# Kernel tuning notes

Hardware: AMD Instinct MI355X
Metric: run time of the kernel (lower is better)

## Reference

```python
import jax, jax.numpy as jnp
import numpy as np

NEG_SLOPE = 0.01  # torch LeakyReLU default
EPS = 1e-5        # torch BatchNorm2d default
N_BINS = 17       # quantization indices 0..16 for uniform [0,1) input


def _bn(x, g, b):
    # training-mode BatchNorm2d: biased batch stats over (B, H, W) per channel
    m = jnp.mean(x, axis=(0, 2, 3), keepdims=True)
    v = jnp.var(x, axis=(0, 2, 3), keepdims=True)
    return (x - m) * jax.lax.rsqrt(v + EPS) * g[None, :, None, None] + b[None, :, None, None]


def _lrelu(x):
    return jnp.where(x >= 0, x, NEG_SLOPE * x)


def _mode_pool_11(idx):
    # idx: int32 (B,C,H,W) quantization bin indices; 11x11 reflect-padded sliding-window mode.
    # Histogram formulation: one-hot over N_BINS, box-sum via 2D integral image, argmax.
    # argmax takes the FIRST max -> smallest modal value, matching torch.mode tie-breaking.
    k = jnp.pad(idx, ((0, 0), (0, 0), (5, 5), (5, 5)), mode='reflect')
    oh = (k[..., None] == jnp.arange(N_BINS, dtype=jnp.int32)).astype(jnp.float32)  # (B,C,Hp,Wp,17)
    I = jnp.cumsum(jnp.cumsum(oh, axis=2), axis=3)
    I = jnp.pad(I, ((0, 0), (0, 0), (1, 0), (1, 0), (0, 0)))
    cnt = I[:, :, 11:, 11:] - I[:, :, :-11, 11:] - I[:, :, 11:, :-11] + I[:, :, :-11, :-11]
    return jnp.argmax(cnt, axis=-1)  # (B,C,H,W) int


def _nearest(x, H, W):
    # torch F.interpolate mode='nearest': src = floor(dst * in / out)
    h, w = x.shape[2], x.shape[3]
    ri = (jnp.arange(H) * h) // H
    ci = (jnp.arange(W) * w) // W
    return x[:, :, ri][:, :, :, ci]


def _conv1x1(x, w, b):
    return jnp.einsum('bchw,oc->bohw', x, w) + b[None, :, None, None]


def reference(x, pw1, pb1, g1, be1, pw2, pb2, g2, be2, dw, sw, gs, bs):
    B, C, H, W = x.shape
    half = pw1.shape[0]
    # quantize: (x*255/16).round() * 16/256 -> index path (round has zero grad anyway)
    idx = jnp.round(x * 255.0 / 16.0).astype(jnp.int32)
    xq = _mode_pool_11(idx).astype(x.dtype) * (16.0 / 256.0)
    # prepare: conv1x1 -> BN -> LeakyReLU, twice
    h1 = _lrelu(_bn(_conv1x1(xq, pw1, pb1), g1, be1))
    prep = _lrelu(_bn(_conv1x1(h1, pw2, pb2), g2, be2))
    score = jnp.zeros((B, 2 * half, H, W), dtype=x.dtype)
    dn = ('NCHW', 'OIHW', 'NCHW')
    previous = prep
    d = prep
    # static pyramid: 512 -> 171 -> 57 -> 19 -> 7 -> 3 -> 1 (shapes known at trace time)
    while min(d.shape[2], d.shape[3]) >= 3:
        d = jax.lax.conv_general_dilated(d, dw, (3, 3), ((1, 1), (1, 1)), dimension_numbers=dn)
        z = _nearest(d, H, W)
        # interleave previous/zoomout per channel: ch 2c=prev[c], 2c+1=zoom[c]
        mix = jnp.stack([previous, z], axis=2).reshape(B, 2 * half, H, W)
        previous = z
        # grouped 1x1 conv: groups=half, 2 in / 2 out channels per group, no bias
        sc = jnp.einsum('bgihw,goi->bgohw', mix.reshape(B, half, 2, H, W), sw).reshape(B, 2 * half, H, W)
        score = score + _lrelu(_bn(sc, gs, bs))
    return score


def setup_inputs() -> dict:
    key = jax.random.key(0)
    ks = jax.random.split(key, 6)
    B, C, H, W = 8, 3, 512, 512
    half = 16
    x = jax.random.uniform(ks[0], (B, C, H, W), dtype=jnp.float32)
    pw1 = 0.1 * jax.random.normal(ks[1], (half, C), dtype=jnp.float32)
    pb1 = jnp.zeros((half,), jnp.float32)
    g1 = jnp.ones((half,), jnp.float32)
    be1 = jnp.zeros((half,), jnp.float32)
    pw2 = 0.1 * jax.random.normal(ks[2], (half, half), dtype=jnp.float32)
    pb2 = jnp.zeros((half,), jnp.float32)
    g2 = jnp.ones((half,), jnp.float32)
    be2 = jnp.zeros((half,), jnp.float32)
    dw = 0.1 * jax.random.normal(ks[3], (half, half, 3, 3), dtype=jnp.float32)
    sw = 0.1 * jax.random.normal(ks[4], (half, 2, 2), dtype=jnp.float32)
    gs = jnp.ones((2 * half,), jnp.float32)
    bs = jnp.zeros((2 * half,), jnp.float32)
    return {'x': x, 'pw1': pw1, 'pb1': pb1, 'g1': g1, 'be1': be1,
            'pw2': pw2, 'pb2': pb2, 'g2': g2, 'be2': be2,
            'dw': dw, 'sw': sw, 'gs': gs, 'bs': bs}
```

## Files before the change

### kernel.cpp

```cpp
#include <hip/hip_runtime.h>
#include <stdint.h>


#define NPX   2097152
#define NINV  (1.0f/2097152.0f)

#define OFF_STATS 0
#define OFF_HIST  16384
#define OFF_LUT   36864
#define OFF_MODE  194560
#define OFF_D1    73594880
#define OFF_D2    88566272
#define OFF_D3    90229760
#define OFF_D4    90414592
#define OFF_D5    90439680
#define OFF_D6    90444288

#define S_PRE1    0
#define S2_PRE1   16
#define S_H1      32
#define S_H1H1    48
#define S_PREP    184
#define S2_PREP   200
#define S_Z1      216
#define S2_Z1     232
#define S_PZ1     248
#define S_LVLBASE 264
#define P_A1      512
#define P_B1      560
#define P_A2      576
#define P_B2      832
#define P_AFF     848

__device__ __forceinline__ uint32_t f2bf(float f) {
  uint32_t u = __float_as_uint(f);
  u += 0x7FFFu + ((u >> 16) & 1u);
  return u >> 16;
}
__device__ __forceinline__ float bf2f(uint32_t u) {
  return __uint_as_float(u << 16);
}

__device__ __forceinline__ float wave_red(float v) {
  v += __shfl_down(v, 32); v += __shfl_down(v, 16); v += __shfl_down(v, 8);
  v += __shfl_down(v, 4);  v += __shfl_down(v, 2);  v += __shfl_down(v, 1);
  return v;
}

template<int K, bool ATOMIC>
__device__ __forceinline__ void block_red(float* acc, float* dst, float* lds) {
  int lane = threadIdx.x & 63, wid = threadIdx.x >> 6;
#pragma unroll
  for (int k = 0; k < K; ++k) {
    float v = wave_red(acc[k]);
    if (lane == 0) lds[wid * K + k] = v;
  }
  __syncthreads();
  if ((int)threadIdx.x < K) {
    float s = lds[threadIdx.x] + lds[K + threadIdx.x] + lds[2 * K + threadIdx.x] + lds[3 * K + threadIdx.x];
    if (ATOMIC) atomicAdd(&dst[threadIdx.x], s);
    else        dst[threadIdx.x] = s;
  }
}

__global__ __launch_bounds__(256) void k_mode(const float* __restrict__ x,
                                              uint8_t* __restrict__ mode) {
  int bx = blockIdx.x;
  int rb = bx & 15, cb = (bx >> 4) & 1, pl = bx >> 5;
  __shared__ uint8_t tile[42][272];
  const float* xp = x + (size_t)pl * 262144;
  int tid = threadIdx.x;
  for (int e = tid; e < 42 * 266; e += 256) {
    int lr = e / 266, lc = e - lr * 266;
    int gr = rb * 32 - 5 + lr; if (gr < 0) gr = -gr; else if (gr > 511) gr = 1022 - gr;
    int gc = cb * 256 - 5 + lc; if (gc < 0) gc = -gc; else if (gc > 511) gc = 1022 - gc;
    float v = xp[gr * 512 + gc];
    tile[lr][lc] = (uint8_t)(int)rintf((v * 255.0f) * 0.0625f);
  }
  __syncthreads();
  int t = tid;
  uint32_t h0 = 0, h1 = 0, h2 = 0, h3 = 0, h4 = 0;
#define ADDV(vv) { int v_ = (vv); uint32_t inc_ = 1u << ((v_ & 3) << 3); int w_ = v_ >> 2; \
    h0 += (w_ == 0) ? inc_ : 0u; h1 += (w_ == 1) ? inc_ : 0u; h2 += (w_ == 2) ? inc_ : 0u; \
    h3 += (w_ == 3) ? inc_ : 0u; h4 += (w_ == 4) ? inc_ : 0u; }
#define SUBV(vv) { int v_ = (vv); uint32_t inc_ = 1u << ((v_ & 3) << 3); int w_ = v_ >> 2; \
    h0 -= (w_ == 0) ? inc_ : 0u; h1 -= (w_ == 1) ? inc_ : 0u; h2 -= (w_ == 2) ? inc_ : 0u; \
    h3 -= (w_ == 3) ? inc_ : 0u; h4 -= (w_ == 4) ? inc_ : 0u; }
#define SCAN_STORE(OI) { uint32_t best_ = h0 & 255u; int bi_ = 0; uint32_t c_; \
    c_ = (h0 >> 8)  & 255u; if (c_ > best_) { best_ = c_; bi_ = 1; } \
    c_ = (h0 >> 16) & 255u; if (c_ > best_) { best_ = c_; bi_ = 2; } \
    c_ = (h0 >> 24);        if (c_ > best_) { best_ = c_; bi_ = 3; } \
    c_ = h1 & 255u;         if (c_ > best_) { best_ = c_; bi_ = 4; } \
    c_ = (h1 >> 8)  & 255u; if (c_ > best_) { best_ = c_; bi_ = 5; } \
    c_ = (h1 >> 16) & 255u; if (c_ > best_) { best_ = c_; bi_ = 6; } \
    c_ = (h1 >> 24);        if (c_ > best_) { best_ = c_; bi_ = 7; } \
    c_ = h2 & 255u;         if (c_ > best_) { best_ = c_; bi_ = 8; } \
    c_ = (h2 >> 8)  & 255u; if (c_ > best_) { best_ = c_; bi_ = 9; } \
    c_ = (h2 >> 16) & 255u; if (c_ > best_) { best_ = c_; bi_ = 10; } \
    c_ = (h2 >> 24);        if (c_ > best_) { best_ = c_; bi_ = 11; } \
    c_ = h3 & 255u;         if (c_ > best_) { best_ = c_; bi_ = 12; } \
    c_ = (h3 >> 8)  & 255u; if (c_ > best_) { best_ = c_; bi_ = 13; } \
    c_ = (h3 >> 16) & 255u; if (c_ > best_) { best_ = c_; bi_ = 14; } \
    c_ = (h3 >> 24);        if (c_ > best_) { best_ = c_; bi_ = 15; } \
    c_ = h4 & 255u;         if (c_ > best_) { best_ = c_; bi_ = 16; } \
    mode[OI] = (uint8_t)bi_; }
#pragma unroll
  for (int dy = 0; dy < 11; ++dy) {
#pragma unroll
    for (int dx = 0; dx < 11; ++dx) ADDV(tile[dy][t + dx]);
  }
  size_t ob = (size_t)pl * 262144 + (size_t)(rb * 32) * 512 + cb * 256 + t;
  SCAN_STORE(ob);
  for (int s = 1; s < 32; ++s) {
#pragma unroll
    for (int dx = 0; dx < 11; ++dx) { SUBV(tile[s - 1][t + dx]); ADDV(tile[s + 10][t + dx]); }
    SCAN_STORE(ob + (size_t)s * 512);
  }
#undef ADDV
#undef SUBV
#undef SCAN_STORE
}

__global__ __launch_bounds__(256) void k_hist(const uint8_t* __restrict__ mode,
                                              uint32_t* __restrict__ hist) {
  __shared__ uint32_t h[4913];
  int tid = threadIdx.x;
  for (int e = tid; e < 4913; e += 256) h[e] = 0;
  __syncthreads();
  int base = blockIdx.x * 8192;
  for (int it = 0; it < 16; ++it) {
    int px = base + it * 512 + tid * 2;
    int b = px >> 18, rem = px & 262143;
    const uint8_t* mp = mode + (size_t)b * 786432 + rem;
    uint32_t m0 = *(const uint16_t*)(mp);
    uint32_t m1 = *(const uint16_t*)(mp + 262144);
    uint32_t m2 = *(const uint16_t*)(mp + 524288);
    int c0 = (int)(m0 & 255u) + 17 * (int)(m1 & 255u) + 289 * (int)(m2 & 255u);
    int c1 = (int)(m0 >> 8)   + 17 * (int)(m1 >> 8)   + 289 * (int)(m2 >> 8);
    atomicAdd(&h[c0], 1u);
    atomicAdd(&h[c1], 1u);
  }
  __syncthreads();
  for (int e = tid; e < 4913; e += 256)
    if (h[e]) atomicAdd(&hist[e], h[e]);
}

__global__ __launch_bounds__(256) void k_build(const uint32_t* __restrict__ hist,
    const float* __restrict__ pw1, const float* __restrict__ pb1,
    const float* __restrict__ g1,  const float* __restrict__ be1,
    const float* __restrict__ pw2, const float* __restrict__ pb2,
    const float* __restrict__ g2,  const float* __restrict__ be2,
    float* __restrict__ stats, uint32_t* __restrict__ lut) {
  __shared__ float red[4 * 152];
  int tid = threadIdx.x;
  {
    float acc[32];
#pragma unroll
    for (int k = 0; k < 32; ++k) acc[k] = 0.f;
    for (int bin = tid; bin < 4913; bin += 256) {
      float w = (float)hist[bin];
      if (w == 0.f) continue;
      int m0 = bin % 17, r = bin / 17;
      int m1 = r % 17, m2 = r / 17;
      float x0 = m0 * 0.0625f, x1 = m1 * 0.0625f, x2 = m2 * 0.0625f;
#pragma unroll
      for (int o = 0; o < 16; ++o) {
        float p = fmaf(pw1[o * 3], x0, fmaf(pw1[o * 3 + 1], x1, fmaf(pw1[o * 3 + 2], x2, pb1[o])));
        acc[o] = fmaf(w, p, acc[o]);
        acc[16 + o] = fmaf(w * p, p, acc[16 + o]);
      }
    }
    block_red<32, false>(acc, stats + S_PRE1, red);
  }
  __syncthreads();
  if (tid < 16) {
    int o = tid;
    float m = stats[S_PRE1 + o] * NINV;
    float var = stats[S2_PRE1 + o] * NINV - m * m;
    float s = g1[o] * rsqrtf(var + 1e-5f);
    stats[P_A1 + o * 3 + 0] = pw1[o * 3 + 0] * s;
    stats[P_A1 + o * 3 + 1] = pw1[o * 3 + 1] * s;
    stats[P_A1 + o * 3 + 2] = pw1[o * 3 + 2] * s;
    stats[P_B1 + o] = (pb1[o] - m) * s + be1[o];
  }
  __syncthreads();
  {
    float acc[152];
#pragma unroll
    for (int k = 0; k < 152; ++k) acc[k] = 0.f;
    for (int bin = tid; bin < 4913; bin += 256) {
      float w = (float)hist[bin];
      if (w == 0.f) continue;
      int m0 = bin % 17, r = bin / 17;
      int m1 = r % 17, m2 = r / 17;
      float x0 = m0 * 0.0625f, x1 = m1 * 0.0625f, x2 = m2 * 0.0625f;
      float h[16];
#pragma unroll
      for (int c = 0; c < 16; ++c) {
        float y = fmaf(stats[P_A1 + c * 3], x0, fmaf(stats[P_A1 + c * 3 + 1], x1,
                  fmaf(stats[P_A1 + c * 3 + 2], x2, stats[P_B1 + c])));
        h[c] = fmaxf(y, 0.01f * y);
        acc[c] = fmaf(w, h[c], acc[c]);
      }
#pragma unroll
      for (int c = 0; c < 16; ++c) {
#pragma unroll
        for (int c2 = c; c2 < 16; ++c2) {
          int idx = 16 * c - (c * (c - 1)) / 2 + (c2 - c);
          acc[16 + idx] = fmaf(w * h[c], h[c2], acc[16 + idx]);
        }
      }
    }
    block_red<152, false>(acc, stats + S_H1, red);
  }
  __syncthreads();
  if (tid < 16) {
    int o = tid;
    float s1 = 0.f;
#pragma unroll
    for (int c = 0; c < 16; ++c) s1 = fmaf(pw2[o * 16 + c], stats[S_H1 + c] * NINV, s1);
    float e2 = 0.f;
#pragma unroll
    for (int c = 0; c < 16; ++c) {
#pragma unroll
      for (int c2 = 0; c2 < 16; ++c2) {
        int lo = c < c2 ? c : c2, hi = c < c2 ? c2 : c;
        int idx = 16 * lo - (lo * (lo - 1)) / 2 + (hi - lo);
        e2 = fmaf(pw2[o * 16 + c] * pw2[o * 16 + c2], stats[S_H1H1 + idx] * NINV, e2);
      }
    }
    float var = e2 - s1 * s1;
    float mean = s1 + pb2[o];
    float s = g2[o] * rsqrtf(var + 1e-5f);
#pragma unroll
    for (int c = 0; c < 16; ++c) stats[P_A2 + o * 16 + c] = pw2[o * 16 + c] * s;
    stats[P_B2 + o] = (pb2[o] - mean) * s + be2[o];
  }
  __syncthreads();
  {
    float acc[32];
#pragma unroll
    for (int k = 0; k < 32; ++k) acc[k] = 0.f;
    for (int bin = tid; bin < 4913; bin += 256) {
      float w = (float)hist[bin];
      int m0 = bin % 17, r = bin / 17;
      int m1 = r % 17, m2 = r / 17;
      float x0 = m0 * 0.0625f, x1 = m1 * 0.0625f, x2 = m2 * 0.0625f;
      float h[16];
#pragma unroll
      for (int c = 0; c < 16; ++c) {
        float y = fmaf(stats[P_A1 + c * 3], x0, fmaf(stats[P_A1 + c * 3 + 1], x1,
                  fmaf(stats[P_A1 + c * 3 + 2], x2, stats[P_B1 + c])));
        h[c] = fmaxf(y, 0.01f * y);
      }
      float p[16];
#pragma unroll
      for (int o = 0; o < 16; ++o) {
        float y = stats[P_B2 + o];
#pragma unroll
        for (int c = 0; c < 16; ++c) y = fmaf(stats[P_A2 + o * 16 + c], h[c], y);
        p[o] = fmaxf(y, 0.01f * y);
        acc[o] = fmaf(w, p[o], acc[o]);
        acc[16 + o] = fmaf(w * p[o], p[o], acc[16 + o]);
      }
#pragma unroll
      for (int d = 0; d < 8; ++d)
        lut[bin * 8 + d] = f2bf(p[2 * d]) | (f2bf(p[2 * d + 1]) << 16);
    }
    block_red<32, false>(acc, stats + S_PREP, red);
  }
}

template<int HIN, int WIN, int HOUT, int WOUT>
__device__ __forceinline__ void conv_body(const float* __restrict__ in,
                                          float* __restrict__ out,
                                          const float* __restrict__ dw, int bx) {
  __shared__ float tile[3][16][WIN + 2];
  int r = bx % HOUT, b = bx / HOUT;
  int tid = threadIdx.x;
  for (int e = tid; e < 48; e += 256) { tile[e / 16][e & 15][0] = 0.f; tile[e / 16][e & 15][WIN + 1] = 0.f; }
  for (int e = tid; e < 3 * 16 * WIN; e += 256) {
    int ky = e / (16 * WIN); int rem = e - ky * (16 * WIN); int ic = rem / WIN; int col = rem - ic * WIN;
    int gr = 3 * r - 1 + ky;
    float v = 0.f;
    if (gr >= 0 && gr < HIN) v = in[((size_t)(b * 16 + ic) * HIN + gr) * WIN + col];
    tile[ky][ic][col + 1] = v;
  }
  __syncthreads();
  int c = tid;
  if (c < WOUT) {
    float acc[16];
#pragma unroll
    for (int o = 0; o < 16; ++o) acc[o] = 0.f;
#pragma unroll
    for (int ic = 0; ic < 16; ++ic) {
      float v[9];
#pragma unroll
      for (int ky = 0; ky < 3; ++ky) {
#pragma unroll
        for (int kx = 0; kx < 3; ++kx) v[ky * 3 + kx] = tile[ky][ic][3 * c + kx];
      }
#pragma unroll
      for (int o = 0; o < 16; ++o) {
        const float* w = dw + (o * 16 + ic) * 9;
#pragma unroll
        for (int tp = 0; tp < 9; ++tp) acc[o] = fmaf(v[tp], w[tp], acc[o]);
      }
    }
#pragma unroll
    for (int o = 0; o < 16; ++o)
      out[((size_t)(b * 16 + o) * HOUT + r) * WOUT + c] = acc[o];
  }
}

template<int HP, int HZ>
__device__ __forceinline__ void pair_body(const float* __restrict__ dp,
                                          const float* __restrict__ dz,
                                          float* __restrict__ dst, int bx) {
  int g = bx & 15, b = (bx >> 4) & 7, jq = bx >> 7;
  const float* dpp = dp + (size_t)(b * 16 + g) * HP * HP;
  const float* dzp = dz + (size_t)(b * 16 + g) * HZ * HZ;
  float a1 = 0.f, a2 = 0.f, a3 = 0.f;
  for (int j = jq * 128; j < jq * 128 + 128; ++j) {
    int r1 = (j * HP) >> 9, r2 = (j * HZ) >> 9;
    const float* rp = dpp + r1 * HP;
    const float* rz = dzp + r2 * HZ;
    for (int i = threadIdx.x; i < 512; i += 256) {
      int c1 = (i * HP) >> 9, c2 = (i * HZ) >> 9;
      float zp = rp[c1], zz = rz[c2];
      a1 += zz; a2 = fmaf(zz, zz, a2); a3 = fmaf(zp, zz, a3);
    }
  }
  a1 = wave_red(a1); a2 = wave_red(a2); a3 = wave_red(a3);
  __shared__ float red[12];
  int lane = threadIdx.x & 63, wid = threadIdx.x >> 6;
  if (!lane) { red[wid * 3] = a1; red[wid * 3 + 1] = a2; red[wid * 3 + 2] = a3; }
  __syncthreads();
  if (threadIdx.x < 3) {
    float s = red[threadIdx.x] + red[3 + threadIdx.x] + red[6 + threadIdx.x] + red[9 + threadIdx.x];
    atomicAdd(&dst[threadIdx.x * 16 + g], s);
  }
}

__device__ __forceinline__ void corr1_body(const uint8_t* __restrict__ mode,
                                           const uint32_t* __restrict__ lut,
                                           const float* __restrict__ d1,
                                           float* __restrict__ stats, int bx) {
  int b = bx >> 6, band = bx & 63;
  float acc[48];
#pragma unroll
  for (int k = 0; k < 48; ++k) acc[k] = 0.f;
  for (int jj = 0; jj < 8; ++jj) {
    int j = band * 8 + jj;
    int r1 = (j * 171) >> 9;
#pragma unroll
    for (int ii = 0; ii < 2; ++ii) {
      int i = (int)threadIdx.x + ii * 256;
      int c1 = (i * 171) >> 9;
      const uint8_t* mp = mode + (size_t)b * 786432 + j * 512 + i;
      int combo = (int)mp[0] + 17 * (int)mp[262144] + 289 * (int)mp[524288];
      const uint4* L = (const uint4*)(lut + combo * 8);
      uint4 q0 = L[0], q1 = L[1];
      uint32_t q[8] = {q0.x, q0.y, q0.z, q0.w, q1.x, q1.y, q1.z, q1.w};
#pragma unroll
      for (int g = 0; g < 16; ++g) {
        float p = bf2f((g & 1) ? (q[g >> 1] >> 16) : (q[g >> 1] & 0xFFFFu));
        float z = d1[((size_t)(b * 16 + g) * 171 + r1) * 171 + c1];
        acc[g] += z; acc[16 + g] = fmaf(z, z, acc[16 + g]); acc[32 + g] = fmaf(p, z, acc[32 + g]);
      }
    }
  }
  __shared__ float red[4 * 48];
  block_red<48, true>(acc, stats + S_Z1, red);
}

__global__ __launch_bounds__(256) void k_conv1g(const uint8_t* __restrict__ mode,
                                                const uint32_t* __restrict__ lut,
                                                float* __restrict__ out,
                                                const float* __restrict__ dw) {
  __shared__ uint16_t tile[3][16][514];
  int bx = blockIdx.x; int r = bx % 171, b = bx / 171;
  int tid = threadIdx.x;
  for (int e = tid; e < 48; e += 256) { tile[e / 16][e & 15][0] = 0; tile[e / 16][e & 15][513] = 0; }
  for (int e = tid; e < 3 * 512; e += 256) {
    int ky = e >> 9, col = e & 511;
    int gr = 3 * r - 1 + ky;
    if (gr < 0 || gr > 511) {
#pragma unroll
      for (int c = 0; c < 16; ++c) tile[ky][c][col + 1] = 0;
    } else {
      const uint8_t* mp = mode + (size_t)b * 786432 + gr * 512 + col;
      int combo = (int)mp[0] + 17 * (int)mp[262144] + 289 * (int)mp[524288];
      const uint4* L = (const uint4*)(lut + combo * 8);
      uint4 q0 = L[0], q1 = L[1];
      uint32_t q[8] = {q0.x, q0.y, q0.z, q0.w, q1.x, q1.y, q1.z, q1.w};
#pragma unroll
      for (int d = 0; d < 8; ++d) {
        tile[ky][2 * d][col + 1]     = (uint16_t)(q[d] & 0xFFFFu);
        tile[ky][2 * d + 1][col + 1] = (uint16_t)(q[d] >> 16);
      }
    }
  }
  __syncthreads();
  int c = tid;
  if (c < 171) {
    float acc[16];
#pragma unroll
    for (int o = 0; o < 16; ++o) acc[o] = 0.f;
#pragma unroll
    for (int ic = 0; ic < 16; ++ic) {
      float v[9];
#pragma unroll
      for (int ky = 0; ky < 3; ++ky) {
#pragma unroll
        for (int kx = 0; kx < 3; ++kx)
          v[ky * 3 + kx] = __uint_as_float(((uint32_t)tile[ky][ic][3 * c + kx]) << 16);
      }
#pragma unroll
      for (int o = 0; o < 16; ++o) {
        const float* w = dw + (o * 16 + ic) * 9;
#pragma unroll
        for (int tp = 0; tp < 9; ++tp) acc[o] = fmaf(v[tp], w[tp], acc[o]);
      }
    }
#pragma unroll
    for (int o = 0; o < 16; ++o)
      out[((size_t)(b * 16 + o) * 171 + r) * 171 + c] = acc[o];
  }
}

__global__ __launch_bounds__(256) void k_conv2_corr1(const float* __restrict__ d1,
    float* __restrict__ d2, const float* __restrict__ dw,
    const uint8_t* __restrict__ mode, const uint32_t* __restrict__ lut,
    float* __restrict__ stats) {
  if ((int)blockIdx.x < 456) conv_body<171, 171, 57, 57>(d1, d2, dw, (int)blockIdx.x);
  else                       corr1_body(mode, lut, d1, stats, (int)blockIdx.x - 456);
}

template<int HIN, int WIN, int HOUT, int WOUT, int NCONV, int HP, int HZ>
__global__ __launch_bounds__(256) void k_conv_pair(const float* __restrict__ cin,
    float* __restrict__ cout, const float* __restrict__ dw,
    const float* __restrict__ dp, const float* __restrict__ dz,
    float* __restrict__ dst) {
  if ((int)blockIdx.x < NCONV) conv_body<HIN, WIN, HOUT, WOUT>(cin, cout, dw, (int)blockIdx.x);
  else                         pair_body<HP, HZ>(dp, dz, dst, (int)blockIdx.x - NCONV);
}

__global__ __launch_bounds__(256) void k_bnL2(float* stats, const float* __restrict__ sw,
    const float* __restrict__ gs, const float* __restrict__ bs,
    const float* __restrict__ d5, const float* __restrict__ d6) {
  __shared__ float l6[3][16][8];
  int t = threadIdx.x;
  if (t < 128) {
    int b = t >> 4, g = t & 15;
    float z6 = d6[b * 16 + g];
    const float* z5 = d5 + (size_t)(b * 16 + g) * 9;
    const float wr[3] = {171.f, 171.f, 170.f};
    float s5 = 0.f;
#pragma unroll
    for (int r = 0; r < 3; ++r)
#pragma unroll
      for (int c = 0; c < 3; ++c) s5 = fmaf(wr[r] * wr[c], z5[r * 3 + c], s5);
    l6[0][g][b] = z6; l6[1][g][b] = z6 * z6; l6[2][g][b] = z6 * s5;
  }
  __syncthreads();
  if (t < 48) {
    int w = t >> 4, g = t & 15;
    float s = 0.f;
#pragma unroll
    for (int b = 0; b < 8; ++b) s += l6[w][g][b];
    stats[S_LVLBASE + 4 * 48 + w * 16 + g] = (w == 2) ? s : s * 262144.f;
  }
  __syncthreads();
  if (t < 192) {
    int lvl = t >> 5, ch = t & 31, g = ch >> 1, o = ch & 1;
    float Sp, Sp2, Sz, Sz2, Spz;
    if (lvl == 0) {
      Sp = stats[S_PREP + g]; Sp2 = stats[S2_PREP + g];
      Sz = stats[S_Z1 + g];   Sz2 = stats[S2_Z1 + g]; Spz = stats[S_PZ1 + g];
    } else {
      int base = S_LVLBASE + (lvl - 1) * 48;
      Sz = stats[base + g]; Sz2 = stats[base + 16 + g]; Spz = stats[base + 32 + g];
      if (lvl == 1) { Sp = stats[S_Z1 + g]; Sp2 = stats[S2_Z1 + g]; }
      else { int pb = S_LVLBASE + (lvl - 2) * 48; Sp = stats[pb + g]; Sp2 = stats[pb + 16 + g]; }
    }
    float mp = Sp * NINV, mz = Sz * NINV;
    float ep2 = Sp2 * NINV, ez2 = Sz2 * NINV, epz = Spz * NINV;
    float w0 = sw[g * 4 + o * 2], w1 = sw[g * 4 + o * 2 + 1];
    float mean = w0 * mp + w1 * mz;
    float e2 = w0 * w0 * ep2 + 2.f * w0 * w1 * epz + w1 * w1 * ez2;
    float var = e2 - mean * mean;
    float s = gs[ch] * rsqrtf(var + 1e-5f);
    float* a = stats + P_AFF + (lvl * 32 + ch) * 3;
    a[0] = s * w0; a[1] = s * w1; a[2] = bs[ch] - mean * s;
  }
}

__global__ __launch_bounds__(256) void k_score(const uint8_t* __restrict__ mode,
    const uint32_t* __restrict__ lut,
    const float* __restrict__ d1, const float* __restrict__ d2, const float* __restrict__ d3,
    const float* __restrict__ d4, const float* __restrict__ d5, const float* __restrict__ d6,
    const float* __restrict__ stats, float* __restrict__ out) {
  __shared__ float zrow[4128];
  __shared__ float aff[576];
  __shared__ uint16_t prow[16][512];
  int bx = blockIdx.x; int b = bx >> 9, j = bx & 511;
  int tid = threadIdx.x;
  {
    const uint8_t* mp = mode + (size_t)b * 786432 + j * 512 + tid * 2;
    uint32_t m0 = *(const uint16_t*)(mp);
    uint32_t m1 = *(const uint16_t*)(mp + 262144);
    uint32_t m2 = *(const uint16_t*)(mp + 524288);
    int ca = (int)(m0 & 255u) + 17 * (int)(m1 & 255u) + 289 * (int)(m2 & 255u);
    int cb = (int)(m0 >> 8)   + 17 * (int)(m1 >> 8)   + 289 * (int)(m2 >> 8);
    const uint4* La = (const uint4*)(lut + ca * 8);
    const uint4* Lb = (const uint4*)(lut + cb * 8);
    uint4 a0 = La[0], a1 = La[1], b0 = Lb[0], b1 = Lb[1];
    uint32_t pa[8] = {a0.x, a0.y, a0.z, a0.w, a1.x, a1.y, a1.z, a1.w};
    uint32_t pb[8] = {b0.x, b0.y, b0.z, b0.w, b1.x, b1.y, b1.z, b1.w};
    uint32_t* pr32 = (uint32_t*)prow;
#pragma unroll
    for (int c = 0; c < 16; ++c) {
      uint32_t lo = (c & 1) ? (pa[c >> 1] >> 16)         : (pa[c >> 1] & 0xFFFFu);
      uint32_t hi = (c & 1) ? (pb[c >> 1] & 0xFFFF0000u) : (pb[c >> 1] << 16);
      pr32[c * 256 + tid] = lo | hi;
    }
  }
  for (int e = tid; e < 576; e += 256) aff[e] = stats[P_AFF + e];
  { int r = (j * 171) >> 9; for (int e = tid; e < 16 * 171; e += 256) { int g = e / 171, c = e - g * 171; zrow[e]        = d1[((size_t)(b * 16 + g) * 171 + r) * 171 + c]; } }
  { int r = (j * 57)  >> 9; for (int e = tid; e < 16 * 57;  e += 256) { int g = e / 57,  c = e - g * 57;  zrow[2736 + e] = d2[((size_t)(b * 16 + g) * 57  + r) * 57  + c]; } }
  { int r = (j * 19)  >> 9; for (int e = tid; e < 16 * 19;  e += 256) { int g = e / 19,  c = e - g * 19;  zrow[3648 + e] = d3[((size_t)(b * 16 + g) * 19  + r) * 19  + c]; } }
  { int r = (j * 7)   >> 9; for (int e = tid; e < 16 * 7;   e += 256) { int g = e / 7,   c = e - g * 7;   zrow[3952 + e] = d4[((size_t)(b * 16 + g) * 7   + r) * 7   + c]; } }
  { int r = (j * 3)   >> 9; for (int e = tid; e < 16 * 3;   e += 256) { int g = e / 3,   c = e - g * 3;   zrow[4064 + e] = d5[((size_t)(b * 16 + g) * 3   + r) * 3   + c]; } }
  { for (int e = tid; e < 16; e += 256) zrow[4112 + e] = d6[b * 16 + e]; }
  __syncthreads();
  int wave = tid >> 6, lane = tid & 63;
#pragma unroll
  for (int gi = 0; gi < 4; ++gi) {
    int g = wave * 4 + gi;
    float A[36];
#pragma unroll
    for (int l = 0; l < 6; ++l) {
#pragma unroll
      for (int q = 0; q < 6; ++q) A[l * 6 + q] = aff[(l * 32 + 2 * g) * 3 + q];
    }
    float z6 = zrow[4112 + g];
    const uint16_t* prow_g = &prow[g][0];
    float* orow = out + ((size_t)(b * 32 + 2 * g) * 512 + j) * 512;
    const float* z1p = zrow + g * 171;
    const float* z2p = zrow + 2736 + g * 57;
    const float* z3p = zrow + 3648 + g * 19;
    const float* z4p = zrow + 3952 + g * 7;
    const float* z5p = zrow + 4064 + g * 3;
#pragma unroll
    for (int k = 0; k < 4; ++k) {
      int i = (lane << 1) + (k << 7);
      uint32_t pv = *(const uint32_t*)(prow_g + i);
      float pA = bf2f(pv & 0xFFFFu), pB = bf2f(pv >> 16);
      int ib = i + 1;
      float za1 = z1p[(i * 171) >> 9], zb1 = z1p[(ib * 171) >> 9];
      float za2 = z2p[(i * 57) >> 9],  zb2 = z2p[(ib * 57) >> 9];
      float za3 = z3p[(i * 19) >> 9],  zb3 = z3p[(ib * 19) >> 9];
      float za4 = z4p[(i * 7) >> 9],   zb4 = z4p[(ib * 7) >> 9];
      float za5 = z5p[(i * 3) >> 9],   zb5 = z5p[(ib * 3) >> 9];
      float o0a = 0.f, o1a = 0.f, prevA = pA;
      float o0b = 0.f, o1b = 0.f, prevB = pB;
#define ST(L, ZA, ZB) { float y_; \
      y_ = fmaf(A[L*6+0], prevA, fmaf(A[L*6+1], (ZA), A[L*6+2])); o0a += fmaxf(y_, 0.01f * y_); \
      y_ = fmaf(A[L*6+3], prevA, fmaf(A[L*6+4], (ZA), A[L*6+5])); o1a += fmaxf(y_, 0.01f * y_); \
      y_ = fmaf(A[L*6+0], prevB, fmaf(A[L*6+1], (ZB), A[L*6+2])); o0b += fmaxf(y_, 0.01f * y_); \
      y_ = fmaf(A[L*6+3], prevB, fmaf(A[L*6+4], (ZB), A[L*6+5])); o1b += fmaxf(y_, 0.01f * y_); \
      prevA = (ZA); prevB = (ZB); }
      ST(0, za1, zb1) ST(1, za2, zb2) ST(2, za3, zb3) ST(3, za4, zb4) ST(4, za5, zb5) ST(5, z6, z6)
#undef ST
      float2 s0 = make_float2(o0a, o0b);
      float2 s1 = make_float2(o1a, o1b);
      *(float2*)(orow + i) = s0;
      *(float2*)(orow + 262144 + i) = s1;
    }
  }
}

extern "C" void kernel_launch(void* const* d_in, const int* in_sizes, int n_in,
                              void* d_out, int out_size, void* d_ws, size_t ws_size,
                              hipStream_t stream) {
  const float* x   = (const float*)d_in[0];
  const float* pw1 = (const float*)d_in[1];
  const float* pb1 = (const float*)d_in[2];
  const float* g1  = (const float*)d_in[3];
  const float* be1 = (const float*)d_in[4];
  const float* pw2 = (const float*)d_in[5];
  const float* pb2 = (const float*)d_in[6];
  const float* g2  = (const float*)d_in[7];
  const float* be2 = (const float*)d_in[8];
  const float* dw  = (const float*)d_in[9];
  const float* sw  = (const float*)d_in[10];
  const float* gs  = (const float*)d_in[11];
  const float* bs  = (const float*)d_in[12];
  char* ws = (char*)d_ws;
  float*    stats = (float*)(ws + OFF_STATS);
  uint32_t* hist  = (uint32_t*)(ws + OFF_HIST);
  uint32_t* lut   = (uint32_t*)(ws + OFF_LUT);
  uint8_t*  mode  = (uint8_t*)(ws + OFF_MODE);
  float* d1 = (float*)(ws + OFF_D1);
  float* d2 = (float*)(ws + OFF_D2);
  float* d3 = (float*)(ws + OFF_D3);
  float* d4 = (float*)(ws + OFF_D4);
  float* d5 = (float*)(ws + OFF_D5);
  float* d6 = (float*)(ws + OFF_D6);
  float* out = (float*)d_out;

  hipMemsetAsync(ws, 0, 36864, stream);
  k_mode<<<768, 256, 0, stream>>>(x, mode);
  k_hist<<<256, 256, 0, stream>>>(mode, hist);
  k_build<<<1, 256, 0, stream>>>(hist, pw1, pb1, g1, be1, pw2, pb2, g2, be2, stats, lut);
  k_conv1g<<<8 * 171, 256, 0, stream>>>(mode, lut, d1, dw);
  k_conv2_corr1<<<456 + 512, 256, 0, stream>>>(d1, d2, dw, mode, lut, stats);
  k_conv_pair<57, 57, 19, 19, 152, 171, 57><<<152 + 512, 256, 0, stream>>>(d2, d3, dw, d1, d2, stats + S_LVLBASE + 0 * 48);
  k_conv_pair<19, 19, 7, 7, 56, 57, 19><<<56 + 512, 256, 0, stream>>>(d3, d4, dw, d2, d3, stats + S_LVLBASE + 1 * 48);
  k_conv_pair<7, 7, 3, 3, 24, 19, 7><<<24 + 512, 256, 0, stream>>>(d4, d5, dw, d3, d4, stats + S_LVLBASE + 2 * 48);
  k_conv_pair<3, 3, 1, 1, 8, 7, 3><<<8 + 512, 256, 0, stream>>>(d5, d6, dw, d4, d5, stats + S_LVLBASE + 3 * 48);
  k_bnL2<<<1, 256, 0, stream>>>(stats, sw, gs, bs, d5, d6);
  k_score<<<4096, 256, 0, stream>>>(mode, lut, d1, d2, d3, d4, d5, d6, stats, out);
}
```

Baseline: 802.8 us.

## Fuse tail pyramid levels into one kernel and fold BN affine into score

Replaces the last three conv_pair launches and the single-block k_bnL2 launch with one k_tail8 kernel. In it, one block per batch runs the small 19->7->3->1 convolutions in shared memory and accumulates the level statistics with shared atomics. The final BN affine computation moves into the prologue of every k_score block, so the separate stats->affine kernel goes away. This cuts the launch count and serial dependencies at the small pyramid levels. In exchange, each of the 4096 score blocks recomputes the affine terms redundantly, and the tail convolutions run on only 8 blocks.

```diff
diff --git a/kernel.cpp b/kernel.cpp
--- a/kernel.cpp
+++ b/kernel.cpp
@@ -30,7 +30,6 @@
 #define P_B1      560
 #define P_A2      576
 #define P_B2      832
-#define P_AFF     848
 
 __device__ __forceinline__ uint32_t f2bf(float f) {
   uint32_t u = __float_as_uint(f);
@@ -437,43 +436,160 @@
   else                       corr1_body(mode, lut, d1, stats, (int)blockIdx.x - 456);
 }
 
-template<int HIN, int WIN, int HOUT, int WOUT, int NCONV, int HP, int HZ>
-__global__ __launch_bounds__(256) void k_conv_pair(const float* __restrict__ cin,
-    float* __restrict__ cout, const float* __restrict__ dw,
-    const float* __restrict__ dp, const float* __restrict__ dz,
-    float* __restrict__ dst) {
-  if ((int)blockIdx.x < NCONV) conv_body<HIN, WIN, HOUT, WOUT>(cin, cout, dw, (int)blockIdx.x);
-  else                         pair_body<HP, HZ>(dp, dz, dst, (int)blockIdx.x - NCONV);
-}
-
-__global__ __launch_bounds__(256) void k_bnL2(float* stats, const float* __restrict__ sw,
+__global__ __launch_bounds__(256) void k_conv3_pair(const float* __restrict__ d2,
+    float* __restrict__ d3, const float* __restrict__ dw,
+    const float* __restrict__ d1, float* __restrict__ stats) {
+  if ((int)blockIdx.x < 152) conv_body<57, 57, 19, 19>(d2, d3, dw, (int)blockIdx.x);
+  else                       pair_body<171, 57>(d1, d2, stats + S_LVLBASE, (int)blockIdx.x - 152);
+}
+
+__global__ __launch_bounds__(256) void k_tail8(const float* __restrict__ d2,
+    const float* __restrict__ d3, float* __restrict__ d4, float* __restrict__ d5,
+    float* __restrict__ d6, const float* __restrict__ dw, float* __restrict__ stats) {
+  int bx = blockIdx.x;
+  if (bx >= 8) { pair_body<57, 19>(d2, d3, stats + S_LVLBASE + 48, bx - 8); return; }
+  __shared__ float s3[16][19][19];
+  __shared__ float s4[16][7][7];
+  __shared__ float s5[16][3][3];
+  __shared__ float s6[16];
+  __shared__ float dwS[2304];
+  __shared__ float acc[144];
+  int tid = threadIdx.x, b = bx;
+  for (int e = tid; e < 2304; e += 256) dwS[e] = dw[e];
+  for (int e = tid; e < 144; e += 256) acc[e] = 0.f;
+  for (int e = tid; e < 16 * 361; e += 256) ((float*)s3)[e] = d3[(size_t)b * 5776 + e];
+  __syncthreads();
+  for (int e = tid; e < 784; e += 256) {
+    int o = e / 49, rc = e - o * 49; int r = rc / 7, c = rc % 7;
+    float a = 0.f;
+#pragma unroll
+    for (int ic = 0; ic < 16; ++ic) {
+      const float* w = dwS + (o * 16 + ic) * 9;
+#pragma unroll
+      for (int ky = 0; ky < 3; ++ky) {
+        int gr = 3 * r - 1 + ky; if (gr < 0 || gr > 18) continue;
+#pragma unroll
+        for (int kx = 0; kx < 3; ++kx) {
+          int gc = 3 * c - 1 + kx; if (gc < 0 || gc > 18) continue;
+          a = fmaf(s3[ic][gr][gc], w[ky * 3 + kx], a);
+        }
+      }
+    }
+    s4[o][r][c] = a; d4[((size_t)(b * 16 + o) * 7 + r) * 7 + c] = a;
+  }
+  __syncthreads();
+  for (int e = tid; e < 784; e += 256) {
+    int g = e & 15, rc = e >> 4; int r2 = rc / 7, c2 = rc % 7;
+    int loZ = (512 * r2 + 6) / 7, hiZ = (512 * (r2 + 1) + 6) / 7;
+    int loC = (512 * c2 + 6) / 7, hiC = (512 * (c2 + 1) + 6) / 7;
+    int rrmin = (loZ * 19) >> 9, rrmax = ((hiZ - 1) * 19) >> 9;
+    int ccmin = (loC * 19) >> 9, ccmax = ((hiC - 1) * 19) >> 9;
+    float z = s4[g][r2][c2];
+    float B = 0.f;
+    for (int rr = rrmin; rr <= rrmax; ++rr) {
+      int loP = (512 * rr + 18) / 19, hiP = (512 * (rr + 1) + 18) / 19;
+      int cntR = min(hiP, hiZ) - max(loP, loZ); if (cntR <= 0) continue;
+      float rowS = 0.f;
+      for (int cc = ccmin; cc <= ccmax; ++cc) {
+        int loQ = (512 * cc + 18) / 19, hiQ = (512 * (cc + 1) + 18) / 19;
+        int cntC = min(hiQ, hiC) - max(loQ, loC); if (cntC <= 0) continue;
+        rowS = fmaf((float)cntC, s3[g][rr][cc], rowS);
+      }
+      B = fmaf((float)cntR, rowS, B);
+    }
+    float wgt = (float)((hiZ - loZ) * (hiC - loC));
+    atomicAdd(&acc[g], wgt * z);
+    atomicAdd(&acc[16 + g], wgt * z * z);
+    atomicAdd(&acc[32 + g], B * z);
+  }
+  for (int e = tid; e < 144; e += 256) {
+    int o = e / 9, rc = e - o * 9; int r = rc / 3, c = rc % 3;
+    float a = 0.f;
+#pragma unroll
+    for (int ic = 0; ic < 16; ++ic) {
+      const float* w = dwS + (o * 16 + ic) * 9;
+#pragma unroll
+      for (int ky = 0; ky < 3; ++ky) {
+        int gr = 3 * r - 1 + ky; if (gr < 0 || gr > 6) continue;
+#pragma unroll
+        for (int kx = 0; kx < 3; ++kx) {
+          int gc = 3 * c - 1 + kx; if (gc < 0 || gc > 6) continue;
+          a = fmaf(s4[ic][gr][gc], w[ky * 3 + kx], a);
+        }
+      }
+    }
+    s5[o][r][c] = a; d5[((size_t)(b * 16 + o) * 3 + r) * 3 + c] = a;
+  }
+  __syncthreads();
+  for (int e = tid; e < 144; e += 256) {
+    int g = e & 15, rc = e >> 4; int r2 = rc / 3, c2 = rc % 3;
+    int loZ = (512 * r2 + 2) / 3, hiZ = (512 * (r2 + 1) + 2) / 3;
+    int loC = (512 * c2 + 2) / 3, hiC = (512 * (c2 + 1) + 2) / 3;
+    int rrmin = (loZ * 7) >> 9, rrmax = ((hiZ - 1) * 7) >> 9;
+    int ccmin = (loC * 7) >> 9, ccmax = ((hiC - 1) * 7) >> 9;
+    float z = s5[g][r2][c2];
+    float B = 0.f;
+    for (int rr = rrmin; rr <= rrmax; ++rr) {
+      int loP = (512 * rr + 6) / 7, hiP = (512 * (rr + 1) + 6) / 7;
+      int cntR = min(hiP, hiZ) - max(loP, loZ); if (cntR <= 0) continue;
+      float rowS = 0.f;
+      for (int cc = ccmin; cc <= ccmax; ++cc) {
+        int loQ = (512 * cc + 6) / 7, hiQ = (512 * (cc + 1) + 6) / 7;
+        int cntC = min(hiQ, hiC) - max(loQ, loC); if (cntC <= 0) continue;
+        rowS = fmaf((float)cntC, s4[g][rr][cc], rowS);
+      }
+      B = fmaf((float)cntR, rowS, B);
+    }
+    float wgt = (float)((hiZ - loZ) * (hiC - loC));
+    atomicAdd(&acc[48 + g], wgt * z);
+    atomicAdd(&acc[64 + g], wgt * z * z);
+    atomicAdd(&acc[80 + g], B * z);
+  }
+  if (tid < 16) {
+    int o = tid; float a = 0.f;
+#pragma unroll
+    for (int ic = 0; ic < 16; ++ic) {
+      const float* w = dwS + (o * 16 + ic) * 9;
+#pragma unroll
+      for (int ky = 1; ky < 3; ++ky)
+#pragma unroll
+        for (int kx = 1; kx < 3; ++kx)
+          a = fmaf(s5[ic][ky - 1][kx - 1], w[ky * 3 + kx], a);
+    }
+    s6[o] = a; d6[b * 16 + o] = a;
+  }
+  __syncthreads();
+  if (tid < 16) {
+    int g = tid; float z6 = s6[g];
+    const float wr3[3] = {171.f, 171.f, 170.f};
+    float s5s = 0.f;
+#pragma unroll
+    for (int r = 0; r < 3; ++r)
+#pragma unroll
+      for (int c = 0; c < 3; ++c) s5s = fmaf(wr3[r] * wr3[c], s5[g][r][c], s5s);
+    acc[96 + g]  += 262144.f * z6;
+    acc[112 + g] += 262144.f * z6 * z6;
+    acc[128 + g] += z6 * s5s;
+  }
+  __syncthreads();
+  for (int e = tid; e < 144; e += 256)
+    atomicAdd(&stats[S_LVLBASE + 96 + e], acc[e]);
+}
+
+__global__ __launch_bounds__(256) void k_score(const uint8_t* __restrict__ mode,
+    const uint32_t* __restrict__ lut,
+    const float* __restrict__ d1, const float* __restrict__ d2, const float* __restrict__ d3,
+    const float* __restrict__ d4, const float* __restrict__ d5, const float* __restrict__ d6,
+    const float* __restrict__ stats, const float* __restrict__ sw,
     const float* __restrict__ gs, const float* __restrict__ bs,
-    const float* __restrict__ d5, const float* __restrict__ d6) {
-  __shared__ float l6[3][16][8];
-  int t = threadIdx.x;
-  if (t < 128) {
-    int b = t >> 4, g = t & 15;
-    float z6 = d6[b * 16 + g];
-    const float* z5 = d5 + (size_t)(b * 16 + g) * 9;
-    const float wr[3] = {171.f, 171.f, 170.f};
-    float s5 = 0.f;
-#pragma unroll
-    for (int r = 0; r < 3; ++r)
-#pragma unroll
-      for (int c = 0; c < 3; ++c) s5 = fmaf(wr[r] * wr[c], z5[r * 3 + c], s5);
-    l6[0][g][b] = z6; l6[1][g][b] = z6 * z6; l6[2][g][b] = z6 * s5;
-  }
-  __syncthreads();
-  if (t < 48) {
-    int w = t >> 4, g = t & 15;
-    float s = 0.f;
-#pragma unroll
-    for (int b = 0; b < 8; ++b) s += l6[w][g][b];
-    stats[S_LVLBASE + 4 * 48 + w * 16 + g] = (w == 2) ? s : s * 262144.f;
-  }
-  __syncthreads();
-  if (t < 192) {
-    int lvl = t >> 5, ch = t & 31, g = ch >> 1, o = ch & 1;
+    float* __restrict__ out) {
+  __shared__ float zrow[4128];
+  __shared__ float aff[576];
+  __shared__ uint16_t prow[16][512];
+  int bx = blockIdx.x; int b = bx >> 9, j = bx & 511;
+  int tid = threadIdx.x;
+  if (tid < 192) {
+    int lvl = tid >> 5, ch = tid & 31, g = ch >> 1, o = ch & 1;
     float Sp, Sp2, Sz, Sz2, Spz;
     if (lvl == 0) {
       Sp = stats[S_PREP + g]; Sp2 = stats[S2_PREP + g];
@@ -491,21 +607,10 @@
     float e2 = w0 * w0 * ep2 + 2.f * w0 * w1 * epz + w1 * w1 * ez2;
     float var = e2 - mean * mean;
     float s = gs[ch] * rsqrtf(var + 1e-5f);
-    float* a = stats + P_AFF + (lvl * 32 + ch) * 3;
-    a[0] = s * w0; a[1] = s * w1; a[2] = bs[ch] - mean * s;
-  }
-}
-
-__global__ __launch_bounds__(256) void k_score(const uint8_t* __restrict__ mode,
-    const uint32_t* __restrict__ lut,
-    const float* __restrict__ d1, const float* __restrict__ d2, const float* __restrict__ d3,
-    const float* __restrict__ d4, const float* __restrict__ d5, const float* __restrict__ d6,
-    const float* __restrict__ stats, float* __restrict__ out) {
-  __shared__ float zrow[4128];
-  __shared__ float aff[576];
-  __shared__ uint16_t prow[16][512];
-  int bx = blockIdx.x; int b = bx >> 9, j = bx & 511;
-  int tid = threadIdx.x;
+    aff[(lvl * 32 + ch) * 3 + 0] = s * w0;
+    aff[(lvl * 32 + ch) * 3 + 1] = s * w1;
+    aff[(lvl * 32 + ch) * 3 + 2] = bs[ch] - mean * s;
+  }
   {
     const uint8_t* mp = mode + (size_t)b * 786432 + j * 512 + tid * 2;
     uint32_t m0 = *(const uint16_t*)(mp);
@@ -526,7 +631,6 @@
       pr32[c * 256 + tid] = lo | hi;
     }
   }
-  for (int e = tid; e < 576; e += 256) aff[e] = stats[P_AFF + e];
   { int r = (j * 171) >> 9; for (int e = tid; e < 16 * 171; e += 256) { int g = e / 171, c = e - g * 171; zrow[e]        = d1[((size_t)(b * 16 + g) * 171 + r) * 171 + c]; } }
   { int r = (j * 57)  >> 9; for (int e = tid; e < 16 * 57;  e += 256) { int g = e / 57,  c = e - g * 57;  zrow[2736 + e] = d2[((size_t)(b * 16 + g) * 57  + r) * 57  + c]; } }
   { int r = (j * 19)  >> 9; for (int e = tid; e < 16 * 19;  e += 256) { int g = e / 19,  c = e - g * 19;  zrow[3648 + e] = d3[((size_t)(b * 16 + g) * 19  + r) * 19  + c]; } }
@@ -616,10 +720,7 @@
   k_build<<<1, 256, 0, stream>>>(hist, pw1, pb1, g1, be1, pw2, pb2, g2, be2, stats, lut);
   k_conv1g<<<8 * 171, 256, 0, stream>>>(mode, lut, d1, dw);
   k_conv2_corr1<<<456 + 512, 256, 0, stream>>>(d1, d2, dw, mode, lut, stats);
-  k_conv_pair<57, 57, 19, 19, 152, 171, 57><<<152 + 512, 256, 0, stream>>>(d2, d3, dw, d1, d2, stats + S_LVLBASE + 0 * 48);
-  k_conv_pair<19, 19, 7, 7, 56, 57, 19><<<56 + 512, 256, 0, stream>>>(d3, d4, dw, d2, d3, stats + S_LVLBASE + 1 * 48);
-  k_conv_pair<7, 7, 3, 3, 24, 19, 7><<<24 + 512, 256, 0, stream>>>(d4, d5, dw, d3, d4, stats + S_LVLBASE + 2 * 48);
-  k_conv_pair<3, 3, 1, 1, 8, 7, 3><<<8 + 512, 256, 0, stream>>>(d5, d6, dw, d4, d5, stats + S_LVLBASE + 3 * 48);
-  k_bnL2<<<1, 256, 0, stream>>>(stats, sw, gs, bs, d5, d6);
-  k_score<<<4096, 256, 0, stream>>>(mode, lut, d1, d2, d3, d4, d5, d6, stats, out);
-}
+  k_conv3_pair<<<152 + 512, 256, 0, stream>>>(d2, d3, dw, d1, stats);
+  k_tail8<<<8 + 512, 256, 0, stream>>>(d2, d3, d4, d5, d6, dw, stats);
+  k_score<<<4096, 256, 0, stream>>>(mode, lut, d1, d2, d3, d4, d5, d6, stats, sw, gs, bs, out);
+}
```

New measurement: 744.5 us. -7.3%, faster.
